# Performance work log

Hardware: AMD Instinct MI355X
Metric: run time of the kernel (lower is better)

Reference implementation:

```python
import jax, jax.numpy as jnp
import numpy as np

N_NODES = 10000
N_EDGES = 160000
N_GRAPHS = 64
X_IN = 128
HID = 64
EDGE_DIM = 16
HEADS = 4
# (in_dim, out_dim_per_head) for the 3 TransformerConv layers (concat=False)
DIMS = [(X_IN, HID), (HID, 2 * HID), (2 * HID, HID)]
WNAMES = [f"{n}{l}" for l in (1, 2, 3) for n in ("wq", "bq", "wk", "bk", "wv", "bv", "we", "ws", "bs")]


def setup_inputs() -> dict:
    key = jax.random.key(0)
    ks = iter(jax.random.split(key, 64))
    inp = {}
    inp["x"] = jax.random.normal(next(ks), (N_NODES, X_IN), jnp.float32)
    inp["edge_index"] = jax.random.randint(next(ks), (2, N_EDGES), 0, N_NODES)
    inp["edge_attr"] = jax.random.normal(next(ks), (N_EDGES, EDGE_DIM), jnp.float32)
    inp["batch"] = jnp.sort(jax.random.randint(next(ks), (N_NODES,), 0, N_GRAPHS))
    for l, (din, dout) in enumerate(DIMS, 1):
        hd = HEADS * dout
        for nm, shape in [("wq", (din, hd)), ("wk", (din, hd)), ("wv", (din, hd)),
                          ("we", (EDGE_DIM, hd)), ("ws", (din, dout))]:
            inp[f"{nm}{l}"] = jax.random.normal(next(ks), shape, jnp.float32) * 0.05
        inp[f"bq{l}"] = jnp.zeros((hd,), jnp.float32)
        inp[f"bk{l}"] = jnp.zeros((hd,), jnp.float32)
        inp[f"bv{l}"] = jnp.zeros((hd,), jnp.float32)
        inp[f"bs{l}"] = jnp.zeros((dout,), jnp.float32)
    return inp


def _transformer_conv(x, src, dst, edge_attr, wq, bq, wk, bk, wv, bv, we, ws, bs, dout):
    """PyG TransformerConv, concat=False, root_weight=True, with edge features."""
    N = x.shape[0]
    q = (x @ wq + bq).reshape(N, HEADS, dout)
    k = (x @ wk + bk).reshape(N, HEADS, dout)
    v = (x @ wv + bv).reshape(N, HEADS, dout)
    e = (edge_attr @ we).reshape(-1, HEADS, dout)  # [E, H, C]
    k_j = k[src] + e                               # edge-conditioned keys
    alpha = jnp.einsum("ehd,ehd->eh", q[dst], k_j) * (1.0 / float(dout) ** 0.5)  # [E, H]
    # numerically stable segment softmax over incoming edges of each dst node
    a_max = jax.ops.segment_max(alpha, dst, num_segments=N)
    ex = jnp.exp(alpha - a_max[dst])
    den = jax.ops.segment_sum(ex, dst, num_segments=N)
    attn = ex / den[dst]
    agg = jax.ops.segment_sum((v[src] + e) * attn[..., None], dst, num_segments=N)  # [N, H, C]
    return agg.mean(axis=1) + x @ ws + bs  # concat=False -> head mean; + skip


def _forward(x, edge_attr, edge_index, batch, params):
    src, dst = edge_index[0], edge_index[1]
    h = x
    for l, (_, dout) in enumerate(DIMS, 1):
        p = [params[f"{n}{l}"] for n in ("wq", "bq", "wk", "bk", "wv", "bv", "we", "ws", "bs")]
        h = jax.nn.elu(_transformer_conv(h, src, dst, edge_attr, *p, dout))
    # global mean pool over graphs
    s = jax.ops.segment_sum(h, batch, num_segments=N_GRAPHS)
    cnt = jax.ops.segment_sum(jnp.ones((h.shape[0], 1), h.dtype), batch, num_segments=N_GRAPHS)
    return s / jnp.maximum(cnt, 1.0)


def reference(x, edge_index, edge_attr, batch,
              wq1, bq1, wk1, bk1, wv1, bv1, we1, ws1, bs1,
              wq2, bq2, wk2, bk2, wv2, bv2, we2, ws2, bs2,
              wq3, bq3, wk3, bk3, wv3, bv3, we3, ws3, bs3):
    params = dict(locals())
    return _forward(x, edge_attr, edge_index, batch, params)
```

## Files before the change

kernel.cpp:

```cpp
#include <hip/hip_runtime.h>
#include <hip/hip_fp16.h>
#include <math.h>

#define N_NODES 10000
#define N_EDGES 160000
#define N_GRAPHS 64

using half8 = __attribute__((ext_vector_type(8))) _Float16;
using floatx4 = __attribute__((ext_vector_type(4))) float;
using h2v = __attribute__((ext_vector_type(2))) _Float16;

template <int NV> struct KW;
template <> struct KW<1> { using T = uint2; };
template <> struct KW<2> { using T = uint4; };

__device__ inline void cvt_kv(const uint2& w, float4* dst) {
  float2 a = __half22float2(*reinterpret_cast<const __half2*>(&w.x));
  float2 b = __half22float2(*reinterpret_cast<const __half2*>(&w.y));
  dst[0] = make_float4(a.x, a.y, b.x, b.y);
}
__device__ inline void cvt_kv(const uint4& w, float4* dst) {
  float2 a = __half22float2(*reinterpret_cast<const __half2*>(&w.x));
  float2 b = __half22float2(*reinterpret_cast<const __half2*>(&w.y));
  float2 c = __half22float2(*reinterpret_cast<const __half2*>(&w.z));
  float2 d = __half22float2(*reinterpret_cast<const __half2*>(&w.w));
  dst[0] = make_float4(a.x, a.y, b.x, b.y);
  dst[1] = make_float4(c.x, c.y, d.x, d.y);
}

#if __has_builtin(__builtin_amdgcn_fdot2)
__device__ inline float dot_qk(const uint2& k, const uint2& q, float c) {
  c = __builtin_amdgcn_fdot2(__builtin_bit_cast(h2v, k.x), __builtin_bit_cast(h2v, q.x), c, false);
  c = __builtin_amdgcn_fdot2(__builtin_bit_cast(h2v, k.y), __builtin_bit_cast(h2v, q.y), c, false);
  return c;
}
__device__ inline float dot_qk(const uint4& k, const uint4& q, float c) {
  c = __builtin_amdgcn_fdot2(__builtin_bit_cast(h2v, k.x), __builtin_bit_cast(h2v, q.x), c, false);
  c = __builtin_amdgcn_fdot2(__builtin_bit_cast(h2v, k.y), __builtin_bit_cast(h2v, q.y), c, false);
  c = __builtin_amdgcn_fdot2(__builtin_bit_cast(h2v, k.z), __builtin_bit_cast(h2v, q.z), c, false);
  c = __builtin_amdgcn_fdot2(__builtin_bit_cast(h2v, k.w), __builtin_bit_cast(h2v, q.w), c, false);
  return c;
}
#else
__device__ inline float dot_qk(const uint2& k, const uint2& q, float c) {
  float4 kk[1], qq[1];
  cvt_kv(k, kk); cvt_kv(q, qq);
  return c + qq[0].x * kk[0].x + qq[0].y * kk[0].y + qq[0].z * kk[0].z + qq[0].w * kk[0].w;
}
__device__ inline float dot_qk(const uint4& k, const uint4& q, float c) {
  float4 kk[2], qq[2];
  cvt_kv(k, kk); cvt_kv(q, qq);
  c += qq[0].x * kk[0].x + qq[0].y * kk[0].y + qq[0].z * kk[0].z + qq[0].w * kk[0].w;
  c += qq[1].x * kk[1].x + qq[1].y * kk[1].y + qq[1].z * kk[1].z + qq[1].w * kk[1].w;
  return c;
}
#endif

__device__ inline int lower_bound(const int* b, int n, int v) {
  int lo = 0, hi = n;
  while (lo < hi) {
    int mid = (lo + hi) >> 1;
    if (b[mid] < v) lo = mid + 1; else hi = mid;
  }
  return lo;
}

template <int K, int HD, int DOUT>
__global__ __launch_bounds__(256) void gemm_mfma(
    const __half* __restrict__ A, const __half* __restrict__ Wp,
    const float* __restrict__ bias, __half* __restrict__ QS,
    __half* __restrict__ KV, int M) {
  constexpr int QSS = HD + 64 + DOUT;
  constexpr int KVS = 2 * HD;
  constexpr int KS = K / 32;
  constexpr int NV = DOUT / 64;
  __shared__ __half st[64][72];
  const int tid = threadIdx.x;
  const int wave = tid >> 6, lane = tid & 63;
  const int quad = lane >> 4, n16 = lane & 15;
  const int row0 = blockIdx.y * 64;
  const int col0 = blockIdx.x * 64;
  const int nblk0 = blockIdx.x * 4;

  const int arow = min(row0 + wave * 16 + n16, M - 1);
  half8 afrag[KS];
#pragma unroll
  for (int s = 0; s < KS; ++s)
    afrag[s] = *reinterpret_cast<const half8*>(A + (size_t)arow * K + s * 32 + quad * 8);

  floatx4 acc[4];
#pragma unroll
  for (int t = 0; t < 4; ++t) {
    acc[t] = (floatx4){0.f, 0.f, 0.f, 0.f};
#pragma unroll
    for (int s = 0; s < KS; ++s) {
      half8 bf = *reinterpret_cast<const half8*>(
          Wp + (((size_t)(nblk0 + t) * KS + s) * 64 + lane) * 8);
      acc[t] = __builtin_amdgcn_mfma_f32_16x16x32_f16(afrag[s], bf, acc[t], 0, 0, 0);
    }
  }

#pragma unroll
  for (int t = 0; t < 4; ++t) {
    float bv = bias[col0 + t * 16 + n16];
#pragma unroll
    for (int r = 0; r < 4; ++r)
      st[wave * 16 + quad * 4 + r][t * 16 + n16] = __float2half(acc[t][r] + bv);
  }
  __syncthreads();

  __half* dp;
  int colb, stride;
  bool kvreg = false;
  if (col0 < HD + 64) {
    dp = QS; colb = col0; stride = QSS;
  } else if (col0 < 3 * HD + 64) {
    dp = KV; colb = col0 - HD - 64; stride = KVS; kvreg = true;
  } else {
    dp = QS; colb = HD + 64 + (col0 - 3 * HD - 64); stride = QSS;
  }
  for (int c = tid; c < 512; c += 256) {
    int r = c >> 3, seg = c & 7;
    int row = row0 + r;
    if (row >= M) continue;
    if (NV == 1 && kvreg) {
      int dfull = colb + seg * 8;
      bool isK = dfull < HD;
      int dd = isK ? dfull : dfull - HD;
      int hh = dd >> 6, d0 = dd & 63;
      int o = hh * 128 + 2 * d0 + (isK ? 0 : 4);
      uint4 w = *reinterpret_cast<const uint4*>(&st[r][seg * 8]);
      *reinterpret_cast<uint2*>(dp + (size_t)row * stride + o) = make_uint2(w.x, w.y);
      *reinterpret_cast<uint2*>(dp + (size_t)row * stride + o + 8) = make_uint2(w.z, w.w);
    } else {
      *reinterpret_cast<uint4*>(dp + (size_t)row * stride + colb + seg * 8) =
          *reinterpret_cast<const uint4*>(&st[r][seg * 8]);
    }
  }
}

__device__ inline void pack_layer(int i, int K, int HD, int DOUT, float scale,
                                  const float* wq, const float* wk,
                                  const float* wv, const float* wsk,
                                  const float* we, const float* bq,
                                  const float* bk, const float* bv,
                                  const float* bs, __half* Wp, float* bcat) {
  const int W = 3 * HD + DOUT + 64;
  const int KS = K / 32;
  if (i < K * W) {
    int j = i & 7, lane = (i >> 3) & 63, fs = i >> 9;
    int nblk = fs / KS, s = fs - nblk * KS;
    int quad = lane >> 4, n = lane & 15;
    int k = s * 32 + quad * 8 + j, c = nblk * 16 + n;
    float v;
    if (c < HD) {
      v = wq[k * HD + c] * scale;
    } else if (c < HD + 64) {
      int gi = c - HD, hh = gi >> 4, d = gi & 15;
      float a = 0.f;
      for (int cc = 0; cc < DOUT; ++cc)
        a += wq[k * HD + hh * DOUT + cc] * we[d * HD + hh * DOUT + cc];
      v = a * scale;
    } else if (c < 2 * HD + 64) {
      v = wk[k * HD + (c - HD - 64)];
    } else if (c < 3 * HD + 64) {
      v = wv[k * HD + (c - 2 * HD - 64)];
    } else {
      v = wsk[k * DOUT + (c - 3 * HD - 64)];
    }
    Wp[i] = __float2half(v);
  } else {
    int c = i - K * W;
    float v;
    if (c < HD) {
      v = bq[c] * scale;
    } else if (c < HD + 64) {
      int gi = c - HD, hh = gi >> 4, d = gi & 15;
      float a = 0.f;
      for (int cc = 0; cc < DOUT; ++cc)
        a += bq[hh * DOUT + cc] * we[d * HD + hh * DOUT + cc];
      v = a * scale;
    } else if (c < 2 * HD + 64) {
      v = bk[c - HD - 64];
    } else if (c < 3 * HD + 64) {
      v = bv[c - 2 * HD - 64];
    } else {
      v = bs[c - 3 * HD - 64];
    }
    bcat[c] = v;
  }
}

#define T1 115584
#define T2 227904
#define T3 343488
#define TCONV (N_NODES * 32)
#define TTOT (T3 + TCONV)
#define NZERO (2 * N_NODES + N_GRAPHS * 64)

__global__ void pack_all(
    const float* wq1, const float* wk1, const float* wv1, const float* ws1,
    const float* we1, const float* bq1, const float* bk1, const float* bv1,
    const float* bs1,
    const float* wq2, const float* wk2, const float* wv2, const float* ws2,
    const float* we2, const float* bq2, const float* bk2, const float* bv2,
    const float* bs2,
    const float* wq3, const float* wk3, const float* wv3, const float* ws3,
    const float* we3, const float* bq3, const float* bk3, const float* bv3,
    const float* bs3,
    __half* W1, float* b1, __half* W2, float* b2, __half* W3, float* b3,
    const float* x, __half* x16, int* cntz, float* doutz) {
  const float SC1 = 0.125f, SC2 = 0.08838834764831845f;
  for (int i = blockIdx.x * blockDim.x + threadIdx.x; i < NZERO;
       i += gridDim.x * blockDim.x) {
    if (i < 2 * N_NODES) cntz[i] = 0;
    else doutz[i - 2 * N_NODES] = 0.f;
  }
  for (int i = blockIdx.x * blockDim.x + threadIdx.x; i < TTOT;
       i += gridDim.x * blockDim.x) {
    if (i < T1)
      pack_layer(i, 128, 256, 64, SC1, wq1, wk1, wv1, ws1, we1, bq1, bk1, bv1, bs1, W1, b1);
    else if (i < T2)
      pack_layer(i - T1, 64, 512, 128, SC2, wq2, wk2, wv2, ws2, we2, bq2, bk2, bv2, bs2, W2, b2);
    else if (i < T3)
      pack_layer(i - T2, 128, 256, 64, SC1, wq3, wk3, wv3, ws3, we3, bq3, bk3, bv3, bs3, W3, b3);
    else {
      int k = i - T3;
      float4 v = reinterpret_cast<const float4*>(x)[k];
      __half2* o = reinterpret_cast<__half2*>(x16) + 2 * k;
      o[0] = __floats2half2_rn(v.x, v.y);
      o[1] = __floats2half2_rn(v.z, v.w);
    }
  }
}

__global__ void count_dst(const int* __restrict__ dst, int* __restrict__ cnt) {
  int e = blockIdx.x * blockDim.x + threadIdx.x;
  if (e < N_EDGES) atomicAdd(&cnt[dst[e]], 1);
}

__global__ __launch_bounds__(1024) void scan_offs(const int* __restrict__ cnt,
                                                  int* __restrict__ offs,
                                                  int* __restrict__ perm,
                                                  const int* __restrict__ batch,
                                                  float* __restrict__ invc) {
  __shared__ int part[1024];
  __shared__ int hist[256], hstart[256], hcur[256];
  const int t = threadIdx.x;
  if (t < N_GRAPHS) {
    int st = lower_bound(batch, N_NODES, t);
    int en = lower_bound(batch, N_NODES, t + 1);
    invc[t] = 1.f / (float)max(en - st, 1);
  }
  const int chunk = (N_NODES + 1023) / 1024;
  const int b = t * chunk;
  const int e = min(N_NODES, b + chunk);
  if (t < 256) { hist[t] = 0; hcur[t] = 0; }
  __syncthreads();
  int s = 0;
  for (int i = b; i < e; ++i) {
    int d = cnt[i];
    s += d;
    atomicAdd(&hist[min(d, 255)], 1);
  }
  part[t] = s;
  __syncthreads();
  for (int off = 1; off < 1024; off <<= 1) {
    int v = (t >= off) ? part[t - off] : 0;
    __syncthreads();
    part[t] += v;
    __syncthreads();
  }
  if (t == 0) {
    int acc = 0;
    for (int bk = 255; bk >= 0; --bk) { hstart[bk] = acc; acc += hist[bk]; }
    offs[N_NODES] = part[1023];
  }
  __syncthreads();
  int pre = (t == 0) ? 0 : part[t - 1];
  for (int i = b; i < e; ++i) {
    offs[i] = pre;
    int d = cnt[i];
    pre += d;
    int bkt = min(d, 255);
    int pos = hstart[bkt] + atomicAdd(&hcur[bkt], 1);
    perm[pos] = i;
  }
}

__global__ void scatter_csr(const int* __restrict__ src, const int* __restrict__ dst,
                            const float* __restrict__ edge_attr,
                            const int* __restrict__ offs, int* __restrict__ cursor,
                            int* __restrict__ csr_src, float* __restrict__ csr_ea) {
  int e = blockIdx.x * blockDim.x + threadIdx.x;
  if (e < N_EDGES) {
    int d = dst[e];
    int pos = offs[d] + atomicAdd(&cursor[d], 1);
    csr_src[pos] = src[e];
    float4* o4 = reinterpret_cast<float4*>(csr_ea + (size_t)pos * 16);
    const float4* s4 = reinterpret_cast<const float4*>(edge_attr + (size_t)e * 16);
    o4[0] = s4[0]; o4[1] = s4[1]; o4[2] = s4[2]; o4[3] = s4[3];
  }
}

template <int DOUT, bool POOL>
__global__ __launch_bounds__(128, 3) void edge_attn(
    const __half* __restrict__ QS, const __half* __restrict__ KV,
    const float* __restrict__ we, const int* __restrict__ csr_src,
    const float* __restrict__ csr_ea, const int* __restrict__ offs,
    const int* __restrict__ perm, const int* __restrict__ batch,
    const float* __restrict__ invc, float* __restrict__ out,
    __half* __restrict__ out16) {
  constexpr int HD = 4 * DOUT;
  constexpr int QSS = HD + 64 + DOUT;
  constexpr int KVS = 2 * HD;
  constexpr int NV = DOUT / 64;
  using KWT = typename KW<NV>::T;

  const int lane = threadIdx.x & 63;
  const int h = lane >> 4, t16 = lane & 15;
  const int n = perm[blockIdx.x * 2 + (threadIdx.x >> 6)];
  const int c0 = t16 * 4 * NV;
  const int kvoff = h * 128 + t16 * 8;

  const __half* base = QS + (size_t)n * QSS;
  KWT qw = *reinterpret_cast<const KWT*>(base + h * DOUT + c0);
  float4 acc[NV];
#pragma unroll
  for (int v = 0; v < NV; ++v) acc[v] = make_float4(0.f, 0.f, 0.f, 0.f);
  const float g = __half2float(base[HD + h * 16 + t16]);

  float lsum = 0.f, tacc = 0.f;

  const int s0 = offs[n], s1 = offs[n + 1];

  float eaA[4], eaB[4], eaC[4];
  uint4 krA[4], vrA[4], krB[4], vrB[4], krC[4], vrC[4];

  for (int cb = s0; cb < s1; cb += 64) {
    const int m = min(64, s1 - cb);
    const int idx = csr_src[cb + min(lane, m - 1)];
    const int ng = m >> 2;

    auto load_grp = [&](int gb, float (&ea)[4], uint4 (&kr)[4], uint4 (&vr)[4]) {
      const int bi = cb + gb;
#pragma unroll
      for (int j = 0; j < 4; ++j) ea[j] = csr_ea[(size_t)(bi + j) * 16 + t16];
#pragma unroll
      for (int j = 0; j < 4; ++j) {
        int sj = __shfl(idx, gb + j);
        const __half* rb = KV + (size_t)sj * KVS + kvoff;
        kr[j] = *reinterpret_cast<const uint4*>(rb);
        if (NV == 2) vr[j] = *reinterpret_cast<const uint4*>(rb + HD);
      }
    };

    auto compute_grp = [&](float (&ea)[4], uint4 (&kr)[4], uint4 (&vr)[4]) {
      float a[4];
#pragma unroll
      for (int j = 0; j < 4; ++j) {
        if (NV == 1)
          a[j] = dot_qk(make_uint2(kr[j].x, kr[j].y),
                        *reinterpret_cast<const uint2*>(&qw), ea[j] * g);
        else
          a[j] = dot_qk(*reinterpret_cast<const uint4*>(&kr[j]),
                        *reinterpret_cast<const uint4*>(&qw), ea[j] * g);
      }
#pragma unroll
      for (int j = 0; j < 4; ++j) {
        a[j] += __shfl_xor(a[j], 1);
        a[j] += __shfl_xor(a[j], 2);
        a[j] += __shfl_xor(a[j], 4);
        a[j] += __shfl_xor(a[j], 8);
      }
      float p0 = __expf(a[0]), p1 = __expf(a[1]);
      float p2 = __expf(a[2]), p3 = __expf(a[3]);
      lsum += p0 + p1 + p2 + p3;
      tacc += p0 * ea[0] + p1 * ea[1] + p2 * ea[2] + p3 * ea[3];
      float pj[4] = {p0, p1, p2, p3};
#pragma unroll
      for (int j = 0; j < 4; ++j) {
        float4 vv[NV];
        if (NV == 1)
          cvt_kv(make_uint2(kr[j].z, kr[j].w), vv);
        else
          cvt_kv(vr[j], vv);
#pragma unroll
        for (int v = 0; v < NV; ++v) {
          acc[v].x += pj[j] * vv[v].x;
          acc[v].y += pj[j] * vv[v].y;
          acc[v].z += pj[j] * vv[v].z;
          acc[v].w += pj[j] * vv[v].w;
        }
      }
    };

    if (ng) {
      load_grp(0, eaA, krA, vrA);
      if (ng > 1) load_grp(4, eaB, krB, vrB);
      int gi = 0;
      for (;;) {
        if (gi + 2 < ng) load_grp((gi + 2) * 4, eaC, krC, vrC);
        compute_grp(eaA, krA, vrA);
        if (++gi >= ng) break;
        if (gi + 2 < ng) load_grp((gi + 2) * 4, eaA, krA, vrA);
        compute_grp(eaB, krB, vrB);
        if (++gi >= ng) break;
        if (gi + 2 < ng) load_grp((gi + 2) * 4, eaB, krB, vrB);
        compute_grp(eaC, krC, vrC);
        if (++gi >= ng) break;
      }
    }

    for (int e = ng * 4; e < m; ++e) {
      int sj = __shfl(idx, e);
      float ea0 = csr_ea[(size_t)(cb + e) * 16 + t16];
      const __half* rb = KV + (size_t)sj * KVS + kvoff;
      uint4 kw = *reinterpret_cast<const uint4*>(rb);
      float a;
      float4 vv[NV];
      if (NV == 1) {
        a = dot_qk(make_uint2(kw.x, kw.y),
                   *reinterpret_cast<const uint2*>(&qw), ea0 * g);
        cvt_kv(make_uint2(kw.z, kw.w), vv);
      } else {
        uint4 vw = *reinterpret_cast<const uint4*>(rb + HD);
        a = dot_qk(kw, *reinterpret_cast<const uint4*>(&qw), ea0 * g);
        cvt_kv(vw, vv);
      }
      a += __shfl_xor(a, 1);
      a += __shfl_xor(a, 2);
      a += __shfl_xor(a, 4);
      a += __shfl_xor(a, 8);
      float p = __expf(a);
      lsum += p;
      tacc += p * ea0;
#pragma unroll
      for (int v = 0; v < NV; ++v) {
        acc[v].x += p * vv[v].x;
        acc[v].y += p * vv[v].y;
        acc[v].z += p * vv[v].z;
        acc[v].w += p * vv[v].w;
      }
    }
  }

  float invl = (lsum > 0.f) ? 1.f / lsum : 0.f;
  float tn = tacc * invl;
  float4 val[NV];
#pragma unroll
  for (int v = 0; v < NV; ++v) {
    val[v].x = acc[v].x * invl; val[v].y = acc[v].y * invl;
    val[v].z = acc[v].z * invl; val[v].w = acc[v].w * invl;
  }
#pragma unroll
  for (int d = 0; d < 16; ++d) {
    float td = __shfl(tn, (lane & 48) | d);
    const float* wb = we + d * HD + h * DOUT + c0;
#pragma unroll
    for (int v = 0; v < NV; ++v) {
      float4 w4 = *reinterpret_cast<const float4*>(wb + 4 * v);
      val[v].x += td * w4.x; val[v].y += td * w4.y;
      val[v].z += td * w4.z; val[v].w += td * w4.w;
    }
  }
#pragma unroll
  for (int v = 0; v < NV; ++v) {
    val[v].x += __shfl_xor(val[v].x, 16); val[v].x += __shfl_xor(val[v].x, 32);
    val[v].y += __shfl_xor(val[v].y, 16); val[v].y += __shfl_xor(val[v].y, 32);
    val[v].z += __shfl_xor(val[v].z, 16); val[v].z += __shfl_xor(val[v].z, 32);
    val[v].w += __shfl_xor(val[v].w, 16); val[v].w += __shfl_xor(val[v].w, 32);
  }
  if (h == 0) {
    KWT sw = *reinterpret_cast<const KWT*>(base + HD + 64 + c0);
    float4 sk[NV];
    cvt_kv(sw, sk);
    float pinv;
    float* gb;
    if (POOL) {
      int gg = batch[n];
      pinv = invc[gg];
      gb = out + gg * 64;
    }
#pragma unroll
    for (int v = 0; v < NV; ++v) {
      float4 o;
      o.x = 0.25f * val[v].x + sk[v].x;
      o.y = 0.25f * val[v].y + sk[v].y;
      o.z = 0.25f * val[v].z + sk[v].z;
      o.w = 0.25f * val[v].w + sk[v].w;
      o.x = (o.x > 0.f) ? o.x : expm1f(o.x);
      o.y = (o.y > 0.f) ? o.y : expm1f(o.y);
      o.z = (o.z > 0.f) ? o.z : expm1f(o.z);
      o.w = (o.w > 0.f) ? o.w : expm1f(o.w);
      if (POOL) {
        float* op = gb + c0 + 4 * v;
        atomicAdd(op + 0, o.x * pinv);
        atomicAdd(op + 1, o.y * pinv);
        atomicAdd(op + 2, o.z * pinv);
        atomicAdd(op + 3, o.w * pinv);
      } else {
        __half2* o16 = reinterpret_cast<__half2*>(out16 + (size_t)n * DOUT + c0 + 4 * v);
        o16[0] = __floats2half2_rn(o.x, o.y);
        o16[1] = __floats2half2_rn(o.z, o.w);
      }
    }
  }
}

extern "C" void kernel_launch(void* const* d_in, const int* in_sizes, int n_in,
                              void* d_out, int out_size, void* d_ws, size_t ws_size,
                              hipStream_t stream) {
  const float* x = (const float*)d_in[0];
  const int* edge_index = (const int*)d_in[1];
  const float* edge_attr = (const float*)d_in[2];
  const int* batch = (const int*)d_in[3];
  const int* srcp = edge_index;
  const int* dstp = edge_index + N_EDGES;

  const bool dict_order = in_sizes[5] > 1024;
  const float *wq[3], *wk[3], *wv[3], *wep[3], *wsk[3], *bq[3], *bk[3], *bv[3], *bs[3];
  for (int L = 0; L < 3; ++L) {
    int b = 4 + L * 9;
    if (dict_order) {
      wq[L] = (const float*)d_in[b + 0];
      wk[L] = (const float*)d_in[b + 1];
      wv[L] = (const float*)d_in[b + 2];
      wep[L] = (const float*)d_in[b + 3];
      wsk[L] = (const float*)d_in[b + 4];
      bq[L] = (const float*)d_in[b + 5];
      bk[L] = (const float*)d_in[b + 6];
      bv[L] = (const float*)d_in[b + 7];
      bs[L] = (const float*)d_in[b + 8];
    } else {
      wq[L] = (const float*)d_in[b + 0];
      bq[L] = (const float*)d_in[b + 1];
      wk[L] = (const float*)d_in[b + 2];
      bk[L] = (const float*)d_in[b + 3];
      wv[L] = (const float*)d_in[b + 4];
      bv[L] = (const float*)d_in[b + 5];
      wep[L] = (const float*)d_in[b + 6];
      wsk[L] = (const float*)d_in[b + 7];
      bs[L] = (const float*)d_in[b + 8];
    }
  }

  char* p = (char*)d_ws;
  __half* qs = (__half*)p;    p += (size_t)N_NODES * 704 * 2;
  __half* kv = (__half*)p;    p += (size_t)N_NODES * 1024 * 2;
  float* h1 = (float*)p;      p += (size_t)N_NODES * 64 * 4;
  __half* x16 = (__half*)p;   p += (size_t)N_NODES * 128 * 2;
  __half* h16 = (__half*)p;   p += (size_t)N_NODES * 128 * 2;
  __half* W1 = (__half*)p;    p += 128 * 896 * 2;
  __half* W2 = (__half*)p;    p += 64 * 1728 * 2;
  __half* W3 = (__half*)p;    p += 128 * 896 * 2;
  float* b1 = (float*)p;      p += 896 * 4;
  float* b2 = (float*)p;      p += 1728 * 4;
  float* b3 = (float*)p;      p += 896 * 4;
  float* invc = (float*)p;    p += 64 * 4;
  float* csr_ea = (float*)p;  p += (size_t)N_EDGES * 16 * 4;
  int* cnt = (int*)p;         p += N_NODES * 4;
  int* cursor = (int*)p;      p += N_NODES * 4;
  int* offs = (int*)p;        p += (N_NODES + 1) * 4;
  int* perm = (int*)p;        p += N_NODES * 4;
  int* csr_src = (int*)p;     p += N_EDGES * 4;

  pack_all<<<1024, 256, 0, stream>>>(
      wq[0], wk[0], wv[0], wsk[0], wep[0], bq[0], bk[0], bv[0], bs[0],
      wq[1], wk[1], wv[1], wsk[1], wep[1], bq[1], bk[1], bv[1], bs[1],
      wq[2], wk[2], wv[2], wsk[2], wep[2], bq[2], bk[2], bv[2], bs[2],
      W1, b1, W2, b2, W3, b3, x, x16, cnt, (float*)d_out);

  count_dst<<<(N_EDGES + 255) / 256, 256, 0, stream>>>(dstp, cnt);
  scan_offs<<<1, 1024, 0, stream>>>(cnt, offs, perm, batch, invc);
  scatter_csr<<<(N_EDGES + 255) / 256, 256, 0, stream>>>(srcp, dstp, edge_attr,
                                                         offs, cursor, csr_src, csr_ea);

  const int MT = (N_NODES + 63) / 64;
  gemm_mfma<128, 256, 64><<<dim3(896 / 64, MT), 256, 0, stream>>>(x16, W1, b1, qs,
                                                                  kv, N_NODES);
  edge_attn<64, false><<<N_NODES / 2, 128, 0, stream>>>(
      qs, kv, wep[0], csr_src, csr_ea, offs, perm, batch, invc, h1, h16);
  gemm_mfma<64, 512, 128><<<dim3(1728 / 64, MT), 256, 0, stream>>>(h16, W2, b2, qs,
                                                                   kv, N_NODES);
  edge_attn<128, false><<<N_NODES / 2, 128, 0, stream>>>(
      qs, kv, wep[1], csr_src, csr_ea, offs, perm, batch, invc, h1, h16);
  gemm_mfma<128, 256, 64><<<dim3(896 / 64, MT), 256, 0, stream>>>(h16, W3, b3, qs,
                                                                  kv, N_NODES);
  edge_attn<64, true><<<N_NODES / 2, 128, 0, stream>>>(
      qs, kv, wep[2], csr_src, csr_ea, offs, perm, batch, invc, (float*)d_out, x16);
}
```

Before: 325.3 us.

## Split edge attention across two waves per node, two heads per wave

The edge attention kernel moves from one wave per node (16 lanes per head, all four heads in one wave) to one 128-thread block per node. Each wave now handles two heads with 32 lanes per head. The two waves combine their head sums through shared memory and a block barrier. The GEMM epilogue drops the interleaved K/V layout for the 64-wide layers and stores K and V contiguously. This doubles the number of blocks and makes each lane's gathers narrower, which should raise memory-level parallelism and spread the work more evenly. In exchange it adds a barrier and an extra shuffle stage, and the K and V gathers now issue separately.

New measurement: 325.3 us (median of 2 runs). No clear change (-0.0%).

```diff
diff --git a/kernel.cpp b/kernel.cpp
--- a/kernel.cpp
+++ b/kernel.cpp
@@ -10,49 +10,39 @@
 using floatx4 = __attribute__((ext_vector_type(4))) float;
 using h2v = __attribute__((ext_vector_type(2))) _Float16;
 
-template <int NV> struct KW;
-template <> struct KW<1> { using T = uint2; };
-template <> struct KW<2> { using T = uint4; };
-
-__device__ inline void cvt_kv(const uint2& w, float4* dst) {
+template <int DL> struct QW2;
+template <> struct QW2<2> { using T = unsigned int; };
+template <> struct QW2<4> { using T = uint2; };
+
+__device__ inline void cvt_v(const unsigned int& w, float* dst) {
+  float2 a = __half22float2(*reinterpret_cast<const __half2*>(&w));
+  dst[0] = a.x; dst[1] = a.y;
+}
+__device__ inline void cvt_v(const uint2& w, float* dst) {
   float2 a = __half22float2(*reinterpret_cast<const __half2*>(&w.x));
   float2 b = __half22float2(*reinterpret_cast<const __half2*>(&w.y));
-  dst[0] = make_float4(a.x, a.y, b.x, b.y);
-}
-__device__ inline void cvt_kv(const uint4& w, float4* dst) {
-  float2 a = __half22float2(*reinterpret_cast<const __half2*>(&w.x));
-  float2 b = __half22float2(*reinterpret_cast<const __half2*>(&w.y));
-  float2 c = __half22float2(*reinterpret_cast<const __half2*>(&w.z));
-  float2 d = __half22float2(*reinterpret_cast<const __half2*>(&w.w));
-  dst[0] = make_float4(a.x, a.y, b.x, b.y);
-  dst[1] = make_float4(c.x, c.y, d.x, d.y);
+  dst[0] = a.x; dst[1] = a.y; dst[2] = b.x; dst[3] = b.y;
 }
 
 #if __has_builtin(__builtin_amdgcn_fdot2)
+__device__ inline float dot_qk(const unsigned int& k, const unsigned int& q, float c) {
+  return __builtin_amdgcn_fdot2(__builtin_bit_cast(h2v, k), __builtin_bit_cast(h2v, q), c, false);
+}
 __device__ inline float dot_qk(const uint2& k, const uint2& q, float c) {
   c = __builtin_amdgcn_fdot2(__builtin_bit_cast(h2v, k.x), __builtin_bit_cast(h2v, q.x), c, false);
   c = __builtin_amdgcn_fdot2(__builtin_bit_cast(h2v, k.y), __builtin_bit_cast(h2v, q.y), c, false);
   return c;
 }
-__device__ inline float dot_qk(const uint4& k, const uint4& q, float c) {
-  c = __builtin_amdgcn_fdot2(__builtin_bit_cast(h2v, k.x), __builtin_bit_cast(h2v, q.x), c, false);
-  c = __builtin_amdgcn_fdot2(__builtin_bit_cast(h2v, k.y), __builtin_bit_cast(h2v, q.y), c, false);
-  c = __builtin_amdgcn_fdot2(__builtin_bit_cast(h2v, k.z), __builtin_bit_cast(h2v, q.z), c, false);
-  c = __builtin_amdgcn_fdot2(__builtin_bit_cast(h2v, k.w), __builtin_bit_cast(h2v, q.w), c, false);
-  return c;
-}
 #else
+__device__ inline float dot_qk(const unsigned int& k, const unsigned int& q, float c) {
+  float kk[2], qq[2];
+  cvt_v(k, kk); cvt_v(q, qq);
+  return c + qq[0] * kk[0] + qq[1] * kk[1];
+}
 __device__ inline float dot_qk(const uint2& k, const uint2& q, float c) {
-  float4 kk[1], qq[1];
-  cvt_kv(k, kk); cvt_kv(q, qq);
-  return c + qq[0].x * kk[0].x + qq[0].y * kk[0].y + qq[0].z * kk[0].z + qq[0].w * kk[0].w;
-}
-__device__ inline float dot_qk(const uint4& k, const uint4& q, float c) {
-  float4 kk[2], qq[2];
-  cvt_kv(k, kk); cvt_kv(q, qq);
-  c += qq[0].x * kk[0].x + qq[0].y * kk[0].y + qq[0].z * kk[0].z + qq[0].w * kk[0].w;
-  c += qq[1].x * kk[1].x + qq[1].y * kk[1].y + qq[1].z * kk[1].z + qq[1].w * kk[1].w;
-  return c;
+  float kk[4], qq[4];
+  cvt_v(k, kk); cvt_v(q, qq);
+  return c + qq[0] * kk[0] + qq[1] * kk[1] + qq[2] * kk[2] + qq[3] * kk[3];
 }
 #endif
 
@@ -73,7 +63,6 @@
   constexpr int QSS = HD + 64 + DOUT;
   constexpr int KVS = 2 * HD;
   constexpr int KS = K / 32;
-  constexpr int NV = DOUT / 64;
   __shared__ __half st[64][72];
   const int tid = threadIdx.x;
   const int wave = tid >> 6, lane = tid & 63;
@@ -111,31 +100,19 @@
 
   __half* dp;
   int colb, stride;
-  bool kvreg = false;
   if (col0 < HD + 64) {
     dp = QS; colb = col0; stride = QSS;
   } else if (col0 < 3 * HD + 64) {
-    dp = KV; colb = col0 - HD - 64; stride = KVS; kvreg = true;
+    dp = KV; colb = col0 - HD - 64; stride = KVS;
   } else {
     dp = QS; colb = HD + 64 + (col0 - 3 * HD - 64); stride = QSS;
   }
   for (int c = tid; c < 512; c += 256) {
     int r = c >> 3, seg = c & 7;
     int row = row0 + r;
-    if (row >= M) continue;
-    if (NV == 1 && kvreg) {
-      int dfull = colb + seg * 8;
-      bool isK = dfull < HD;
-      int dd = isK ? dfull : dfull - HD;
-      int hh = dd >> 6, d0 = dd & 63;
-      int o = hh * 128 + 2 * d0 + (isK ? 0 : 4);
-      uint4 w = *reinterpret_cast<const uint4*>(&st[r][seg * 8]);
-      *reinterpret_cast<uint2*>(dp + (size_t)row * stride + o) = make_uint2(w.x, w.y);
-      *reinterpret_cast<uint2*>(dp + (size_t)row * stride + o + 8) = make_uint2(w.z, w.w);
-    } else {
+    if (row < M)
       *reinterpret_cast<uint4*>(dp + (size_t)row * stride + colb + seg * 8) =
           *reinterpret_cast<const uint4*>(&st[r][seg * 8]);
-    }
   }
 }
 
@@ -304,7 +281,7 @@
 }
 
 template <int DOUT, bool POOL>
-__global__ __launch_bounds__(128, 3) void edge_attn(
+__global__ __launch_bounds__(128) void edge_attn(
     const __half* __restrict__ QS, const __half* __restrict__ KV,
     const float* __restrict__ we, const int* __restrict__ csr_src,
     const float* __restrict__ csr_ea, const int* __restrict__ offs,
@@ -314,64 +291,65 @@
   constexpr int HD = 4 * DOUT;
   constexpr int QSS = HD + 64 + DOUT;
   constexpr int KVS = 2 * HD;
-  constexpr int NV = DOUT / 64;
-  using KWT = typename KW<NV>::T;
-
-  const int lane = threadIdx.x & 63;
-  const int h = lane >> 4, t16 = lane & 15;
-  const int n = perm[blockIdx.x * 2 + (threadIdx.x >> 6)];
-  const int c0 = t16 * 4 * NV;
-  const int kvoff = h * 128 + t16 * 8;
+  constexpr int DL = DOUT / 32;
+  using QT = typename QW2<DL>::T;
+
+  __shared__ float lds[2][DOUT];
+
+  const int tid = threadIdx.x;
+  const int hp = tid >> 6;
+  const int lane = tid & 63;
+  const int h_local = lane >> 5;
+  const int head = hp * 2 + h_local;
+  const int t32 = lane & 31;
+  const int c0 = t32 * DL;
+  const int n = perm[blockIdx.x];
 
   const __half* base = QS + (size_t)n * QSS;
-  KWT qw = *reinterpret_cast<const KWT*>(base + h * DOUT + c0);
-  float4 acc[NV];
-#pragma unroll
-  for (int v = 0; v < NV; ++v) acc[v] = make_float4(0.f, 0.f, 0.f, 0.f);
-  const float g = __half2float(base[HD + h * 16 + t16]);
-
+  QT qw = *reinterpret_cast<const QT*>(base + head * DOUT + c0);
+  const float gg = (t32 < 16) ? __half2float(base[HD + head * 16 + t32]) : 0.f;
+  const int eoff = t32 & 15;
+
+  float acc[DL];
+#pragma unroll
+  for (int i = 0; i < DL; ++i) acc[i] = 0.f;
   float lsum = 0.f, tacc = 0.f;
 
   const int s0 = offs[n], s1 = offs[n + 1];
+  const int kvoff = head * DOUT + c0;
 
   float eaA[4], eaB[4], eaC[4];
-  uint4 krA[4], vrA[4], krB[4], vrB[4], krC[4], vrC[4];
+  QT krA[4], vrA[4], krB[4], vrB[4], krC[4], vrC[4];
 
   for (int cb = s0; cb < s1; cb += 64) {
     const int m = min(64, s1 - cb);
     const int idx = csr_src[cb + min(lane, m - 1)];
     const int ng = m >> 2;
 
-    auto load_grp = [&](int gb, float (&ea)[4], uint4 (&kr)[4], uint4 (&vr)[4]) {
+    auto load_grp = [&](int gb, float (&ea)[4], QT (&kr)[4], QT (&vr)[4]) {
       const int bi = cb + gb;
 #pragma unroll
-      for (int j = 0; j < 4; ++j) ea[j] = csr_ea[(size_t)(bi + j) * 16 + t16];
+      for (int j = 0; j < 4; ++j) ea[j] = csr_ea[(size_t)(bi + j) * 16 + eoff];
 #pragma unroll
       for (int j = 0; j < 4; ++j) {
         int sj = __shfl(idx, gb + j);
         const __half* rb = KV + (size_t)sj * KVS + kvoff;
-        kr[j] = *reinterpret_cast<const uint4*>(rb);
-        if (NV == 2) vr[j] = *reinterpret_cast<const uint4*>(rb + HD);
+        kr[j] = *reinterpret_cast<const QT*>(rb);
+        vr[j] = *reinterpret_cast<const QT*>(rb + HD);
       }
     };
 
-    auto compute_grp = [&](float (&ea)[4], uint4 (&kr)[4], uint4 (&vr)[4]) {
+    auto compute_grp = [&](float (&ea)[4], QT (&kr)[4], QT (&vr)[4]) {
       float a[4];
 #pragma unroll
-      for (int j = 0; j < 4; ++j) {
-        if (NV == 1)
-          a[j] = dot_qk(make_uint2(kr[j].x, kr[j].y),
-                        *reinterpret_cast<const uint2*>(&qw), ea[j] * g);
-        else
-          a[j] = dot_qk(*reinterpret_cast<const uint4*>(&kr[j]),
-                        *reinterpret_cast<const uint4*>(&qw), ea[j] * g);
-      }
+      for (int j = 0; j < 4; ++j) a[j] = dot_qk(kr[j], qw, ea[j] * gg);
 #pragma unroll
       for (int j = 0; j < 4; ++j) {
         a[j] += __shfl_xor(a[j], 1);
         a[j] += __shfl_xor(a[j], 2);
         a[j] += __shfl_xor(a[j], 4);
         a[j] += __shfl_xor(a[j], 8);
+        a[j] += __shfl_xor(a[j], 16);
       }
       float p0 = __expf(a[0]), p1 = __expf(a[1]);
       float p2 = __expf(a[2]), p3 = __expf(a[3]);
@@ -380,18 +358,10 @@
       float pj[4] = {p0, p1, p2, p3};
 #pragma unroll
       for (int j = 0; j < 4; ++j) {
-        float4 vv[NV];
-        if (NV == 1)
-          cvt_kv(make_uint2(kr[j].z, kr[j].w), vv);
-        else
-          cvt_kv(vr[j], vv);
-#pragma unroll
-        for (int v = 0; v < NV; ++v) {
-          acc[v].x += pj[j] * vv[v].x;
-          acc[v].y += pj[j] * vv[v].y;
-          acc[v].z += pj[j] * vv[v].z;
-          acc[v].w += pj[j] * vv[v].w;
-        }
+        float vv[DL];
+        cvt_v(vr[j], vv);
+#pragma unroll
+        for (int i = 0; i < DL; ++i) acc[i] += pj[j] * vv[i];
       }
     };
 
@@ -414,96 +384,66 @@
 
     for (int e = ng * 4; e < m; ++e) {
       int sj = __shfl(idx, e);
-      float ea0 = csr_ea[(size_t)(cb + e) * 16 + t16];
+      float ea0 = csr_ea[(size_t)(cb + e) * 16 + eoff];
       const __half* rb = KV + (size_t)sj * KVS + kvoff;
-      uint4 kw = *reinterpret_cast<const uint4*>(rb);
-      float a;
-      float4 vv[NV];
-      if (NV == 1) {
-        a = dot_qk(make_uint2(kw.x, kw.y),
-                   *reinterpret_cast<const uint2*>(&qw), ea0 * g);
-        cvt_kv(make_uint2(kw.z, kw.w), vv);
-      } else {
-        uint4 vw = *reinterpret_cast<const uint4*>(rb + HD);
-        a = dot_qk(kw, *reinterpret_cast<const uint4*>(&qw), ea0 * g);
-        cvt_kv(vw, vv);
-      }
+      QT kw = *reinterpret_cast<const QT*>(rb);
+      QT vw = *reinterpret_cast<const QT*>(rb + HD);
+      float a = dot_qk(kw, qw, ea0 * gg);
       a += __shfl_xor(a, 1);
       a += __shfl_xor(a, 2);
       a += __shfl_xor(a, 4);
       a += __shfl_xor(a, 8);
+      a += __shfl_xor(a, 16);
       float p = __expf(a);
       lsum += p;
       tacc += p * ea0;
-#pragma unroll
-      for (int v = 0; v < NV; ++v) {
-        acc[v].x += p * vv[v].x;
-        acc[v].y += p * vv[v].y;
-        acc[v].z += p * vv[v].z;
-        acc[v].w += p * vv[v].w;
-      }
+      float vv[DL];
+      cvt_v(vw, vv);
+#pragma unroll
+      for (int i = 0; i < DL; ++i) acc[i] += p * vv[i];
     }
   }
 
   float invl = (lsum > 0.f) ? 1.f / lsum : 0.f;
   float tn = tacc * invl;
-  float4 val[NV];
-#pragma unroll
-  for (int v = 0; v < NV; ++v) {
-    val[v].x = acc[v].x * invl; val[v].y = acc[v].y * invl;
-    val[v].z = acc[v].z * invl; val[v].w = acc[v].w * invl;
-  }
+  float val[DL];
+#pragma unroll
+  for (int i = 0; i < DL; ++i) val[i] = acc[i] * invl;
 #pragma unroll
   for (int d = 0; d < 16; ++d) {
-    float td = __shfl(tn, (lane & 48) | d);
-    const float* wb = we + d * HD + h * DOUT + c0;
-#pragma unroll
-    for (int v = 0; v < NV; ++v) {
-      float4 w4 = *reinterpret_cast<const float4*>(wb + 4 * v);
-      val[v].x += td * w4.x; val[v].y += td * w4.y;
-      val[v].z += td * w4.z; val[v].w += td * w4.w;
-    }
-  }
-#pragma unroll
-  for (int v = 0; v < NV; ++v) {
-    val[v].x += __shfl_xor(val[v].x, 16); val[v].x += __shfl_xor(val[v].x, 32);
-    val[v].y += __shfl_xor(val[v].y, 16); val[v].y += __shfl_xor(val[v].y, 32);
-    val[v].z += __shfl_xor(val[v].z, 16); val[v].z += __shfl_xor(val[v].z, 32);
-    val[v].w += __shfl_xor(val[v].w, 16); val[v].w += __shfl_xor(val[v].w, 32);
-  }
-  if (h == 0) {
-    KWT sw = *reinterpret_cast<const KWT*>(base + HD + 64 + c0);
-    float4 sk[NV];
-    cvt_kv(sw, sk);
-    float pinv;
-    float* gb;
+    float td = __shfl(tn, (lane & 32) | d);
+    const float* wb = we + d * HD + head * DOUT + c0;
+#pragma unroll
+    for (int i = 0; i < DL; ++i) val[i] += td * wb[i];
+  }
+#pragma unroll
+  for (int i = 0; i < DL; ++i) val[i] += __shfl_xor(val[i], 32);
+  if (lane < 32) {
+#pragma unroll
+    for (int i = 0; i < DL; ++i) lds[hp][c0 + i] = val[i];
+  }
+  __syncthreads();
+  if (hp == 0 && lane < 32) {
+    float sk[DL];
+    QT sw = *reinterpret_cast<const QT*>(base + HD + 64 + c0);
+    cvt_v(sw, sk);
+    float o[DL];
+#pragma unroll
+    for (int i = 0; i < DL; ++i) {
+      float tot = 0.25f * (val[i] + lds[1][c0 + i]) + sk[i];
+      o[i] = (tot > 0.f) ? tot : expm1f(tot);
+    }
     if (POOL) {
-      int gg = batch[n];
-      pinv = invc[gg];
-      gb = out + gg * 64;
-    }
-#pragma unroll
-    for (int v = 0; v < NV; ++v) {
-      float4 o;
-      o.x = 0.25f * val[v].x + sk[v].x;
-      o.y = 0.25f * val[v].y + sk[v].y;
-      o.z = 0.25f * val[v].z + sk[v].z;
-      o.w = 0.25f * val[v].w + sk[v].w;
-      o.x = (o.x > 0.f) ? o.x : expm1f(o.x);
-      o.y = (o.y > 0.f) ? o.y : expm1f(o.y);
-      o.z = (o.z > 0.f) ? o.z : expm1f(o.z);
-      o.w = (o.w > 0.f) ? o.w : expm1f(o.w);
-      if (POOL) {
-        float* op = gb + c0 + 4 * v;
-        atomicAdd(op + 0, o.x * pinv);
-        atomicAdd(op + 1, o.y * pinv);
-        atomicAdd(op + 2, o.z * pinv);
-        atomicAdd(op + 3, o.w * pinv);
-      } else {
-        __half2* o16 = reinterpret_cast<__half2*>(out16 + (size_t)n * DOUT + c0 + 4 * v);
-        o16[0] = __floats2half2_rn(o.x, o.y);
-        o16[1] = __floats2half2_rn(o.z, o.w);
-      }
+      int gg2 = batch[n];
+      float pinv = invc[gg2];
+      float* op = out + gg2 * 64 + c0;
+#pragma unroll
+      for (int i = 0; i < DL; ++i) atomicAdd(op + i, o[i] * pinv);
+    } else {
+      __half2* o16 = reinterpret_cast<__half2*>(out16 + (size_t)n * DOUT + c0);
+#pragma unroll
+      for (int i = 0; i < DL / 2; ++i)
+        o16[i] = __floats2half2_rn(o[2 * i], o[2 * i + 1]);
     }
   }
 }
@@ -579,14 +519,14 @@
   const int MT = (N_NODES + 63) / 64;
   gemm_mfma<128, 256, 64><<<dim3(896 / 64, MT), 256, 0, stream>>>(x16, W1, b1, qs,
                                                                   kv, N_NODES);
-  edge_attn<64, false><<<N_NODES / 2, 128, 0, stream>>>(
+  edge_attn<64, false><<<N_NODES, 128, 0, stream>>>(
       qs, kv, wep[0], csr_src, csr_ea, offs, perm, batch, invc, h1, h16);
   gemm_mfma<64, 512, 128><<<dim3(1728 / 64, MT), 256, 0, stream>>>(h16, W2, b2, qs,
                                                                    kv, N_NODES);
-  edge_attn<128, false><<<N_NODES / 2, 128, 0, stream>>>(
+  edge_attn<128, false><<<N_NODES, 128, 0, stream>>>(
       qs, kv, wep[1], csr_src, csr_ea, offs, perm, batch, invc, h1, h16);
   gemm_mfma<128, 256, 64><<<dim3(896 / 64, MT), 256, 0, stream>>>(h16, W3, b3, qs,
                                                                   kv, N_NODES);
-  edge_attn<64, true><<<N_NODES / 2, 128, 0, stream>>>(
+  edge_attn<64, true><<<N_NODES, 128, 0, stream>>>(
       qs, kv, wep[2], csr_src, csr_ea, offs, perm, batch, invc, (float*)d_out, x16);
 }
```
